# Kernel tuning notes

Measured on AMD Instinct MI355X. Metric: run time of the kernel, lower is better.

## Reference

```python
import jax, jax.numpy as jnp
import numpy as np

B, N, C, H = 8, 2048, 512, 8
D = C // H  # head_dim = 64

def rope(t):
    # t: (B, H, T, D); rotate even/odd interleaved pairs
    T = t.shape[2]
    inv_freq = 1.0 / (10000.0 ** (jnp.arange(0, D, 2, dtype=t.dtype) / D))  # (D/2,)
    pos = jnp.arange(T, dtype=t.dtype)
    freqs = pos[:, None] * inv_freq[None, :]            # (T, D/2)
    cos, sin = jnp.cos(freqs), jnp.sin(freqs)           # broadcast over (B,H)
    t_un = t[..., 0::2]
    t_ev = t[..., 1::2]
    r_un = t_un * cos - t_ev * sin
    r_ev = t_un * sin + t_ev * cos
    # interleave back: (..., D/2, 2) -> (..., D)
    return jnp.stack([r_un, r_ev], axis=-1).reshape(t.shape)

def setup_inputs() -> dict:
    key = jax.random.key(0)
    k1, k2, k3, k4 = jax.random.split(key, 4)
    x = jax.random.normal(k1, (B, N, C), dtype=jnp.float32)
    mask = jax.random.normal(k2, (B, N), dtype=jnp.float32)
    W_qkv = jax.random.normal(k3, (3 * C, C), dtype=jnp.float32) * (1.0 / np.sqrt(C))
    W_proj = jax.random.normal(k4, (C, C), dtype=jnp.float32) * (1.0 / np.sqrt(C))
    b_proj = jnp.zeros((C,), dtype=jnp.float32)
    return {"x": x, "mask": mask, "W_qkv": W_qkv, "W_proj": W_proj,
            "b_proj": b_proj, "num_cls_token": 1}

def reference(x, mask, W_qkv, W_proj, b_proj, num_cls_token):
    scale = D ** (-0.5)
    qkv = jnp.einsum('bnc,fc->bnf', x, W_qkv)             # (B,N,3C)
    qkv = qkv.reshape(B, N, 3, H, D).transpose(2, 0, 3, 1, 4)  # (3,B,H,N,D)
    q, k, v = qkv[0], qkv[1], qkv[2]
    nc = num_cls_token
    if nc > 0:
        q = jnp.concatenate([q[:, :, :nc], rope(q[:, :, nc:])], axis=2)
        k = jnp.concatenate([k[:, :, :nc], rope(k[:, :, nc:])], axis=2)
    else:
        q, k = rope(q), rope(k)
    attn = jnp.einsum('bhnd,bhmd->bhnm', q * scale, k)    # (B,H,N,N)
    attn = attn + mask[:, None, None, :] + mask[:, None, :, None]
    attn = jax.nn.softmax(attn, axis=-1)
    out = jnp.einsum('bhnm,bhmd->bhnd', attn, v)          # (B,H,N,D)
    out = out.transpose(0, 2, 1, 3).reshape(B, N, C)
    return out @ W_proj.T + b_proj
```

## Files before the change

### kernel.cpp

```cpp
#include <hip/hip_runtime.h>
#include <cmath>

#define BB 8
#define NN 2048
#define CC 512
#define HH 8
#define DD 64
#define FF 1536
#define MM (BB*NN)

typedef _Float16 half_t;
typedef __attribute__((ext_vector_type(8))) _Float16 half8;
typedef __attribute__((ext_vector_type(4))) _Float16 half4;
typedef __attribute__((ext_vector_type(4))) float floatx4;
typedef __attribute__((ext_vector_type(16))) float floatx16;
typedef __attribute__((ext_vector_type(4))) float fx4;

#define LOG2E 1.44269504088896f

typedef const __attribute__((address_space(1))) unsigned int* gas_ptr;
typedef __attribute__((address_space(3))) unsigned int* las_ptr;
__device__ __forceinline__ void gld16(const half_t* g, half_t* l) {
  __builtin_amdgcn_global_load_lds((gas_ptr)g, (las_ptr)l, 16, 0, 0);
}

__global__ __launch_bounds__(256) void cvt_kernel(
    const float* __restrict__ s, half_t* __restrict__ d, int n8) {
  int i = blockIdx.x * 256 + threadIdx.x;
  if (i < n8) {
    float4 a = ((const float4*)s)[i * 2], b = ((const float4*)s)[i * 2 + 1];
    half8 h;
    h[0] = (half_t)a.x; h[1] = (half_t)a.y; h[2] = (half_t)a.z; h[3] = (half_t)a.w;
    h[4] = (half_t)b.x; h[5] = (half_t)b.y; h[6] = (half_t)b.z; h[7] = (half_t)b.w;
    ((half8*)d)[i] = h;
  }
}

__global__ __launch_bounds__(256) void qkv_mfma_kernel(
    const half_t* __restrict__ Ah,
    const half_t* __restrict__ Bh,
    const int*   __restrict__ ncp,
    half_t* __restrict__ Qh, half_t* __restrict__ Kh, half_t* __restrict__ Vt)
{
  __shared__ union {
    struct { half_t A[128 * 32]; half_t B[128 * 32]; } s;
    half_t T[4][64 * 68];
  } sm;

  const int tid  = threadIdx.x;
  const int wave = tid >> 6, lane = tid & 63;
  const int L15  = lane & 15, quad = lane >> 4;
  const int wm = (wave & 1) * 64, wn = (wave >> 1) * 64;
  const int m0 = blockIdx.x * 128;
  const int f0 = blockIdx.y * 128;

  const int srow = lane >> 2;
  const int scolh = (lane & 3) * 8;
  const half_t* Ag = Ah + (size_t)(m0 + wave * 16 + srow) * CC + scolh;
  const half_t* Bg = Bh + (size_t)(f0 + wave * 16 + srow) * CC + scolh;
  half_t* Al = &sm.s.A[(wave * 16) * 32];
  half_t* Bl = &sm.s.B[(wave * 16) * 32];

  floatx4 acc[4][4];
#pragma unroll
  for (int i = 0; i < 4; ++i)
#pragma unroll
    for (int j = 0; j < 4; ++j) acc[i][j] = (floatx4){0.f, 0.f, 0.f, 0.f};

  for (int k0 = 0; k0 < CC; k0 += 32) {
    __syncthreads();
    gld16(Ag + k0,            Al);
    gld16(Ag + k0 + 64 * CC,  Al + 64 * 32);
    gld16(Bg + k0,            Bl);
    gld16(Bg + k0 + 64 * CC,  Bl + 64 * 32);
    __syncthreads();
    half8 af[4], bf[4];
#pragma unroll
    for (int mi = 0; mi < 4; ++mi)
      af[mi] = *(const half8*)&sm.s.A[(wm + mi * 16 + L15) * 32 + quad * 8];
#pragma unroll
    for (int ni = 0; ni < 4; ++ni)
      bf[ni] = *(const half8*)&sm.s.B[(wn + ni * 16 + L15) * 32 + quad * 8];
#pragma unroll
    for (int mi = 0; mi < 4; ++mi)
#pragma unroll
      for (int ni = 0; ni < 4; ++ni)
        acc[mi][ni] = __builtin_amdgcn_mfma_f32_16x16x32_f16(af[mi], bf[ni], acc[mi][ni], 0, 0, 0);
  }

  const int which = f0 >> 9;
  const int b     = m0 >> 11;
  const int n_base = (m0 & 2047) + wm;

  if (which < 2) {
    const int nc = *ncp;
    half_t* dst = which ? Kh : Qh;
    const float qscale = which ? 1.0f : (0.125f * LOG2E);
#pragma unroll
    for (int ni = 0; ni < 4; ++ni) {
      const int f = f0 + wn + ni * 16 + L15;
      const int h = (f >> 6) & 7;
      const int d = f & 63;
      const float invf = __powf(10000.0f, -(float)(d & ~1) * (1.0f / 64.0f));
      const float sgn = (d & 1) ? 1.0f : -1.0f;
#pragma unroll
      for (int mi = 0; mi < 4; ++mi)
#pragma unroll
        for (int r = 0; r < 4; ++r) {
          const int n = n_base + mi * 16 + quad * 4 + r;
          float v = acc[mi][ni][r];
          float p = __shfl_xor(v, 1, 64);
          if (n >= nc) {
            float sv, cv;
            __sincosf((float)(n - nc) * invf, &sv, &cv);
            v = v * cv + sgn * p * sv;
          }
          dst[(((size_t)(b * HH + h) * NN + n) << 6) + d] = (half_t)(v * qscale);
        }
    }
  } else {
    __syncthreads();
#pragma unroll
    for (int ni = 0; ni < 4; ++ni)
#pragma unroll
      for (int mi = 0; mi < 4; ++mi)
#pragma unroll
        for (int r = 0; r < 4; ++r)
          sm.T[wave][(ni * 16 + L15) * 68 + mi * 16 + quad * 4 + r] = (half_t)acc[mi][ni][r];
    __syncthreads();
    const int h = ((f0 + wn) >> 6) & 7;
    const size_t gbase = ((size_t)(b * HH + h) * DD + lane) * NN + n_base;
#pragma unroll
    for (int c = 0; c < 8; ++c)
      *(half8*)(Vt + gbase + c * 8) = *(const half8*)&sm.T[wave][lane * 68 + c * 8];
  }
}

#define EXP2_OFF 4.3280851f
__global__ __launch_bounds__(256, 4) void flash_mfma_kernel(
    const half_t* __restrict__ Qh,
    const half_t* __restrict__ Kh,
    const half_t* __restrict__ Vt,
    const float*  __restrict__ mask,
    half_t* __restrict__ O)
{
  __shared__ half_t KV[2][2][64 * 64];

  const int tid  = threadIdx.x;
  const int wave = tid >> 6;
  const int lane = tid & 63;
  const int l31  = lane & 31;
  const int hi   = lane >> 5;
  const int l7   = lane & 7;

  const int bid  = blockIdx.x;
  const int xcd  = bid & 7;
  const int slot = bid >> 3;
  const int qt   = slot & 15;
  const int head = (slot >> 4) * 8 + xcd;
  const int b    = head >> 3;
  const int h    = head & 7;

  const half_t* Kt_base = Kh + ((((size_t)b * HH + h) * NN) << 6);
  const half_t* Vt_base = Vt + (((size_t)b * HH + h) * DD) * NN;

  half8 qf[4];
  {
    const half_t* Qp =
        Qh + ((((size_t)b * HH + h) * NN + qt * 128 + wave * 32 + l31) << 6) + hi * 8;
#pragma unroll
    for (int kd = 0; kd < 4; ++kd) qf[kd] = *(const half8*)(Qp + kd * 16);
  }

  const int r8  = lane >> 3;
  const int dof = ((l7 ^ r8) << 3);
  const half_t* kbase = Kt_base + (((size_t)(wave * 16 + r8)) << 6) + dof;
  const half_t* vbase = Vt_base + (size_t)(wave * 16 + r8) * NN + dof;

  int adK[4], adV[4];
#pragma unroll
  for (int c = 0; c < 4; ++c) {
    adK[c] = l31 * 128 + ((((c << 1) | hi) ^ l7) << 4);
    adV[c] = 8192 + l31 * 128 + ((((c << 1) | hi) ^ l7) << 4);
  }
  const char* L = (const char*)KV;

  floatx16 acc[2];
#pragma unroll
  for (int dt = 0; dt < 2; ++dt)
#pragma unroll
    for (int r = 0; r < 16; ++r) acc[dt][r] = 0.f;
  float l_part = 0.f;

  const float* mkb = mask + (size_t)b * NN + hi * 4;

#define STAGE(c, koff, voff)                                                  \
  {                                                                           \
    gld16(kbase + (koff),          &KV[c][0][wave * 1024]);                   \
    gld16(kbase + (koff) + 512,    &KV[c][0][wave * 1024 + 512]);             \
    gld16(vbase + (voff),          &KV[c][1][wave * 1024]);                   \
    gld16(vbase + (voff) + 8 * NN, &KV[c][1][wave * 1024 + 512]);             \
  }

#define COMPUTE(c, moff)                                                      \
  _Pragma("unroll")                                                           \
  for (int t = 0; t < 2; ++t) {                                               \
    fx4 m4[4];                                                                \
    _Pragma("unroll")                                                         \
    for (int r2 = 0; r2 < 4; ++r2)                                            \
      m4[r2] = *(const fx4*)(mkb + (moff) + t * 32 + r2 * 8);                 \
    floatx16 S;                                                               \
    _Pragma("unroll") for (int r = 0; r < 16; ++r) S[r] = 0.f;                \
    __builtin_amdgcn_s_setprio(1);                                            \
    _Pragma("unroll")                                                         \
    for (int kd = 0; kd < 4; ++kd) {                                          \
      half8 kf = *(const half8*)(L + (adK[kd] + (c) * 16384 + t * 4096));     \
      S = __builtin_amdgcn_mfma_f32_32x32x16_f16(kf, qf[kd], S, 0, 0, 0);     \
    }                                                                         \
    __builtin_amdgcn_s_setprio(0);                                            \
    _Pragma("unroll")                                                         \
    for (int r = 0; r < 16; ++r) {                                            \
      float p = __builtin_amdgcn_exp2f(fmaf(m4[r >> 2][r & 3], LOG2E, S[r] - EXP2_OFF)); \
      l_part += p;                                                            \
      S[r] = p;                                                               \
    }                                                                         \
    unsigned W[4][2];                                                         \
    _Pragma("unroll")                                                         \
    for (int r2 = 0; r2 < 4; ++r2)                                            \
      _Pragma("unroll")                                                       \
      for (int u = 0; u < 2; ++u) {                                           \
        union { half_t hh[2]; unsigned w; } pk;                               \
        pk.hh[0] = (half_t)S[r2 * 4 + 2 * u];                                 \
        pk.hh[1] = (half_t)S[r2 * 4 + 2 * u + 1];                             \
        W[r2][u] = pk.w;                                                      \
      }                                                                       \
    _Pragma("unroll")                                                         \
    for (int ksl = 0; ksl < 2; ++ksl) {                                       \
      unsigned A0 = W[2 * ksl][0],     A1 = W[2 * ksl][1];                    \
      unsigned B0 = W[2 * ksl + 1][0], B1 = W[2 * ksl + 1][1];                \
      unsigned pA0 = __shfl_xor(A0, 32, 64), pA1 = __shfl_xor(A1, 32, 64);    \
      unsigned pB0 = __shfl_xor(B0, 32, 64), pB1 = __shfl_xor(B1, 32, 64);    \
      union { unsigned u4[4]; half8 v; } pw;                                  \
      pw.u4[0] = hi ? pB0 : A0;                                               \
      pw.u4[1] = hi ? pB1 : A1;                                               \
      pw.u4[2] = hi ? B0 : pA0;                                               \
      pw.u4[3] = hi ? B1 : pA1;                                               \
      const int ks = t * 2 + ksl;                                             \
      __builtin_amdgcn_s_setprio(1);                                          \
      _Pragma("unroll")                                                       \
      for (int dt = 0; dt < 2; ++dt) {                                        \
        half8 vf = *(const half8*)(L + (adV[ks] + (c) * 16384 + dt * 4096));  \
        acc[dt] = __builtin_amdgcn_mfma_f32_32x32x16_f16(pw.v, vf, acc[dt], 0, 0, 0); \
      }                                                                       \
      __builtin_amdgcn_s_setprio(0);                                          \
    }                                                                         \
  }

  STAGE(0, 0, 0)
  STAGE(1, 4096, 64)
  asm volatile("s_waitcnt vmcnt(4)");
  __builtin_amdgcn_s_barrier();
  __builtin_amdgcn_sched_barrier(0);
  kbase += 8192; vbase += 128;

#pragma unroll 1
  for (int kt2 = 0; kt2 < 15; ++kt2) {
    COMPUTE(0, 0)
    __builtin_amdgcn_sched_barrier(0);
    __builtin_amdgcn_s_barrier();
    STAGE(0, 0, 0)
    asm volatile("s_waitcnt vmcnt(4)");
    __builtin_amdgcn_s_barrier();
    __builtin_amdgcn_sched_barrier(0);

    COMPUTE(1, 64)
    __builtin_amdgcn_sched_barrier(0);
    __builtin_amdgcn_s_barrier();
    STAGE(1, 4096, 64)
    asm volatile("s_waitcnt vmcnt(4)");
    __builtin_amdgcn_s_barrier();
    __builtin_amdgcn_sched_barrier(0);

    kbase += 8192; vbase += 128;
    mkb += 128;
  }

  COMPUTE(0, 0)
  asm volatile("s_waitcnt vmcnt(0)");
  __builtin_amdgcn_s_barrier();
  __builtin_amdgcn_sched_barrier(0);
  COMPUTE(1, 64)

#undef STAGE
#undef COMPUTE

  l_part += __shfl_xor(l_part, 32, 64);

  const size_t orow = (size_t)b * NN + qt * 128 + wave * 32;
#pragma unroll
  for (int r = 0; r < 16; ++r) {
    const int ql  = (r & 3) + 8 * (r >> 2) + 4 * hi;
    const float iv = 1.0f / __shfl(l_part, ql, 64);
    const size_t ro = ((orow + ql) << 9) + (h << 6) + l31;
    O[ro]      = (half_t)(acc[0][r] * iv);
    O[ro + 32] = (half_t)(acc[1][r] * iv);
  }
}

__global__ __launch_bounds__(256) void proj_mfma_kernel(
    const half_t* __restrict__ Ah,
    const half_t* __restrict__ Bh,
    const float* __restrict__ bias,
    float* __restrict__ out)
{
  __shared__ half_t As[128 * 32];
  __shared__ half_t Bs[128 * 32];

  const int tid  = threadIdx.x;
  const int wave = tid >> 6, lane = tid & 63;
  const int L15  = lane & 15, quad = lane >> 4;
  const int wm = (wave & 1) * 64, wn = (wave >> 1) * 64;
  const int m0 = blockIdx.x * 128;
  const int f0 = blockIdx.y * 128;

  const int srow = lane >> 2;
  const int scolh = (lane & 3) * 8;
  const half_t* Ag = Ah + (size_t)(m0 + wave * 16 + srow) * CC + scolh;
  const half_t* Bg = Bh + (size_t)(f0 + wave * 16 + srow) * CC + scolh;
  half_t* Al = &As[(wave * 16) * 32];
  half_t* Bl = &Bs[(wave * 16) * 32];

  floatx4 acc[4][4];
#pragma unroll
  for (int i = 0; i < 4; ++i)
#pragma unroll
    for (int j = 0; j < 4; ++j) acc[i][j] = (floatx4){0.f, 0.f, 0.f, 0.f};

  for (int k0 = 0; k0 < CC; k0 += 32) {
    __syncthreads();
    gld16(Ag + k0,           Al);
    gld16(Ag + k0 + 64 * CC, Al + 64 * 32);
    gld16(Bg + k0,           Bl);
    gld16(Bg + k0 + 64 * CC, Bl + 64 * 32);
    __syncthreads();
    half8 af[4], bf[4];
#pragma unroll
    for (int mi = 0; mi < 4; ++mi)
      af[mi] = *(const half8*)&As[(wm + mi * 16 + L15) * 32 + quad * 8];
#pragma unroll
    for (int ni = 0; ni < 4; ++ni)
      bf[ni] = *(const half8*)&Bs[(wn + ni * 16 + L15) * 32 + quad * 8];
#pragma unroll
    for (int mi = 0; mi < 4; ++mi)
#pragma unroll
      for (int ni = 0; ni < 4; ++ni)
        acc[mi][ni] = __builtin_amdgcn_mfma_f32_16x16x32_f16(af[mi], bf[ni], acc[mi][ni], 0, 0, 0);
  }

#pragma unroll
  for (int ni = 0; ni < 4; ++ni) {
    const int f = f0 + wn + ni * 16 + L15;
    const float bv = bias[f];
#pragma unroll
    for (int mi = 0; mi < 4; ++mi)
#pragma unroll
      for (int r = 0; r < 4; ++r)
        out[(size_t)(m0 + wm + mi * 16 + quad * 4 + r) * CC + f] = acc[mi][ni][r] + bv;
  }
}

extern "C" void kernel_launch(void* const* d_in, const int* in_sizes, int n_in,
                              void* d_out, int out_size, void* d_ws, size_t ws_size,
                              hipStream_t stream) {
  const float* x     = (const float*)d_in[0];
  const float* mask  = (const float*)d_in[1];
  const float* Wqkv  = (const float*)d_in[2];
  const float* Wproj = (const float*)d_in[3];
  const float* bproj = (const float*)d_in[4];
  const int*   ncp   = (const int*)d_in[5];
  float* out = (float*)d_out;

  const size_t per = (size_t)BB * HH * NN * DD;
  half_t* xh  = (half_t*)d_ws;
  half_t* Wqh = xh + (size_t)MM * CC;
  half_t* Wph = Wqh + (size_t)FF * CC;
  half_t* Qh  = Wph + (size_t)CC * CC;
  half_t* Kh  = Qh + per;
  half_t* Vt  = Kh + per;
  half_t* Oh  = Vt + per;

  cvt_kernel<<<dim3(MM * CC / 8 / 256), 256, 0, stream>>>(x, xh, MM * CC / 8);
  cvt_kernel<<<dim3(FF * CC / 8 / 256), 256, 0, stream>>>(Wqkv, Wqh, FF * CC / 8);
  cvt_kernel<<<dim3(CC * CC / 8 / 256), 256, 0, stream>>>(Wproj, Wph, CC * CC / 8);

  qkv_mfma_kernel<<<dim3(MM / 128, FF / 128), 256, 0, stream>>>(xh, Wqh, ncp, Qh, Kh, Vt);
  flash_mfma_kernel<<<dim3(BB * HH * (NN / 128)), 256, 0, stream>>>(Qh, Kh, Vt, mask, Oh);
  proj_mfma_kernel<<<dim3(MM / 128, CC / 128), 256, 0, stream>>>(Oh, Wph, bproj, out);
}
```

Before: 270.8 us.

## Split flash attention KV range across two wave groups and precompute RoPE table

The flash kernel now runs 512 threads per block: two groups of four waves each process alternating 64-key tiles of the KV sequence for the same 128 queries. Their partial accumulators and row sums are merged through LDS at the end, in exchange for single-buffered staging per group with full vmcnt(0) waits. This doubles the waves per query tile to raise parallelism and latency hiding. Separately, RoPE cos/sin values are precomputed into a table by a small kernel, replacing per-element sincos/pow in the QKV epilogue with table loads.

```diff
diff --git a/kernel.cpp b/kernel.cpp
--- a/kernel.cpp
+++ b/kernel.cpp
@@ -36,10 +36,20 @@
   }
 }
 
+__global__ __launch_bounds__(256) void rope_tab_kernel(float2* __restrict__ tab) {
+  int i = blockIdx.x * 256 + threadIdx.x;
+  int p = i >> 5, j = i & 31;
+  float ang = (float)p * __powf(10000.0f, -(float)(2 * j) * (1.0f / 64.0f));
+  float sv, cv;
+  __sincosf(ang, &sv, &cv);
+  tab[i] = make_float2(cv, sv);
+}
+
 __global__ __launch_bounds__(256) void qkv_mfma_kernel(
     const half_t* __restrict__ Ah,
     const half_t* __restrict__ Bh,
     const int*   __restrict__ ncp,
+    const float2* __restrict__ tab,
     half_t* __restrict__ Qh, half_t* __restrict__ Kh, half_t* __restrict__ Vt)
 {
   __shared__ union {
@@ -101,8 +111,8 @@
       const int f = f0 + wn + ni * 16 + L15;
       const int h = (f >> 6) & 7;
       const int d = f & 63;
-      const float invf = __powf(10000.0f, -(float)(d & ~1) * (1.0f / 64.0f));
       const float sgn = (d & 1) ? 1.0f : -1.0f;
+      const float2* tj = tab + (d >> 1);
 #pragma unroll
       for (int mi = 0; mi < 4; ++mi)
 #pragma unroll
@@ -111,9 +121,8 @@
           float v = acc[mi][ni][r];
           float p = __shfl_xor(v, 1, 64);
           if (n >= nc) {
-            float sv, cv;
-            __sincosf((float)(n - nc) * invf, &sv, &cv);
-            v = v * cv + sgn * p * sv;
+            float2 cs = tj[(size_t)(n - nc) * 32];
+            v = v * cs.x + sgn * p * cs.y;
           }
           dst[(((size_t)(b * HH + h) * NN + n) << 6) + d] = (half_t)(v * qscale);
         }
@@ -137,7 +146,7 @@
 }
 
 #define EXP2_OFF 4.3280851f
-__global__ __launch_bounds__(256, 4) void flash_mfma_kernel(
+__global__ __launch_bounds__(512, 8) void flash_mfma_kernel(
     const half_t* __restrict__ Qh,
     const half_t* __restrict__ Kh,
     const half_t* __restrict__ Vt,
@@ -145,9 +154,12 @@
     half_t* __restrict__ O)
 {
   __shared__ half_t KV[2][2][64 * 64];
+  __shared__ float  Ll[128];
 
   const int tid  = threadIdx.x;
   const int wave = tid >> 6;
+  const int wg   = wave & 3;
+  const int grp  = wave >> 2;
   const int lane = tid & 63;
   const int l31  = lane & 31;
   const int hi   = lane >> 5;
@@ -167,21 +179,21 @@
   half8 qf[4];
   {
     const half_t* Qp =
-        Qh + ((((size_t)b * HH + h) * NN + qt * 128 + wave * 32 + l31) << 6) + hi * 8;
+        Qh + ((((size_t)b * HH + h) * NN + qt * 128 + wg * 32 + l31) << 6) + hi * 8;
 #pragma unroll
     for (int kd = 0; kd < 4; ++kd) qf[kd] = *(const half8*)(Qp + kd * 16);
   }
 
   const int r8  = lane >> 3;
   const int dof = ((l7 ^ r8) << 3);
-  const half_t* kbase = Kt_base + (((size_t)(wave * 16 + r8)) << 6) + dof;
-  const half_t* vbase = Vt_base + (size_t)(wave * 16 + r8) * NN + dof;
+  const half_t* kbase = Kt_base + (((size_t)(grp * 64 + wg * 16 + r8)) << 6) + dof;
+  const half_t* vbase = Vt_base + (size_t)(wg * 16 + r8) * NN + grp * 64 + dof;
 
   int adK[4], adV[4];
 #pragma unroll
   for (int c = 0; c < 4; ++c) {
-    adK[c] = l31 * 128 + ((((c << 1) | hi) ^ l7) << 4);
-    adV[c] = 8192 + l31 * 128 + ((((c << 1) | hi) ^ l7) << 4);
+    adK[c] = grp * 16384 + l31 * 128 + ((((c << 1) | hi) ^ l7) << 4);
+    adV[c] = grp * 16384 + 8192 + l31 * 128 + ((((c << 1) | hi) ^ l7) << 4);
   }
   const char* L = (const char*)KV;
 
@@ -192,29 +204,30 @@
     for (int r = 0; r < 16; ++r) acc[dt][r] = 0.f;
   float l_part = 0.f;
 
-  const float* mkb = mask + (size_t)b * NN + hi * 4;
-
-#define STAGE(c, koff, voff)                                                  \
+  const float* mkb = mask + (size_t)b * NN + grp * 64 + hi * 4;
+
+#define STAGE_KV()                                                            \
   {                                                                           \
-    gld16(kbase + (koff),          &KV[c][0][wave * 1024]);                   \
-    gld16(kbase + (koff) + 512,    &KV[c][0][wave * 1024 + 512]);             \
-    gld16(vbase + (voff),          &KV[c][1][wave * 1024]);                   \
-    gld16(vbase + (voff) + 8 * NN, &KV[c][1][wave * 1024 + 512]);             \
-  }
-
-#define COMPUTE(c, moff)                                                      \
+    gld16(kbase,          &KV[grp][0][wg * 1024]);                            \
+    gld16(kbase + 512,    &KV[grp][0][wg * 1024 + 512]);                      \
+    gld16(vbase,          &KV[grp][1][wg * 1024]);                            \
+    gld16(vbase + 8 * NN, &KV[grp][1][wg * 1024 + 512]);                      \
+    kbase += 8192; vbase += 128;                                              \
+  }
+
+#define COMPUTE()                                                             \
   _Pragma("unroll")                                                           \
   for (int t = 0; t < 2; ++t) {                                               \
     fx4 m4[4];                                                                \
     _Pragma("unroll")                                                         \
     for (int r2 = 0; r2 < 4; ++r2)                                            \
-      m4[r2] = *(const fx4*)(mkb + (moff) + t * 32 + r2 * 8);                 \
+      m4[r2] = *(const fx4*)(mkb + t * 32 + r2 * 8);                          \
     floatx16 S;                                                               \
     _Pragma("unroll") for (int r = 0; r < 16; ++r) S[r] = 0.f;                \
     __builtin_amdgcn_s_setprio(1);                                            \
     _Pragma("unroll")                                                         \
     for (int kd = 0; kd < 4; ++kd) {                                          \
-      half8 kf = *(const half8*)(L + (adK[kd] + (c) * 16384 + t * 4096));     \
+      half8 kf = *(const half8*)(L + (adK[kd] + t * 4096));                   \
       S = __builtin_amdgcn_mfma_f32_32x32x16_f16(kf, qf[kd], S, 0, 0, 0);     \
     }                                                                         \
     __builtin_amdgcn_s_setprio(0);                                            \
@@ -249,61 +262,62 @@
       __builtin_amdgcn_s_setprio(1);                                          \
       _Pragma("unroll")                                                       \
       for (int dt = 0; dt < 2; ++dt) {                                        \
-        half8 vf = *(const half8*)(L + (adV[ks] + (c) * 16384 + dt * 4096));  \
+        half8 vf = *(const half8*)(L + (adV[ks] + dt * 4096));                \
         acc[dt] = __builtin_amdgcn_mfma_f32_32x32x16_f16(pw.v, vf, acc[dt], 0, 0, 0); \
       }                                                                       \
       __builtin_amdgcn_s_setprio(0);                                          \
     }                                                                         \
   }
 
-  STAGE(0, 0, 0)
-  STAGE(1, 4096, 64)
-  asm volatile("s_waitcnt vmcnt(4)");
-  __builtin_amdgcn_s_barrier();
-  __builtin_amdgcn_sched_barrier(0);
-  kbase += 8192; vbase += 128;
-
-#pragma unroll 1
-  for (int kt2 = 0; kt2 < 15; ++kt2) {
-    COMPUTE(0, 0)
-    __builtin_amdgcn_sched_barrier(0);
-    __builtin_amdgcn_s_barrier();
-    STAGE(0, 0, 0)
-    asm volatile("s_waitcnt vmcnt(4)");
-    __builtin_amdgcn_s_barrier();
-    __builtin_amdgcn_sched_barrier(0);
-
-    COMPUTE(1, 64)
-    __builtin_amdgcn_sched_barrier(0);
-    __builtin_amdgcn_s_barrier();
-    STAGE(1, 4096, 64)
-    asm volatile("s_waitcnt vmcnt(4)");
-    __builtin_amdgcn_s_barrier();
-    __builtin_amdgcn_sched_barrier(0);
-
-    kbase += 8192; vbase += 128;
-    mkb += 128;
-  }
-
-  COMPUTE(0, 0)
+  STAGE_KV()
   asm volatile("s_waitcnt vmcnt(0)");
   __builtin_amdgcn_s_barrier();
   __builtin_amdgcn_sched_barrier(0);
-  COMPUTE(1, 64)
-
-#undef STAGE
+
+#pragma unroll 1
+  for (int s = 0; s < 15; ++s) {
+    COMPUTE()
+    __builtin_amdgcn_sched_barrier(0);
+    __builtin_amdgcn_s_barrier();
+    STAGE_KV()
+    asm volatile("s_waitcnt vmcnt(0)");
+    __builtin_amdgcn_s_barrier();
+    __builtin_amdgcn_sched_barrier(0);
+    mkb += 128;
+  }
+  COMPUTE()
+
+#undef STAGE_KV
 #undef COMPUTE
 
+  __builtin_amdgcn_s_barrier();
   l_part += __shfl_xor(l_part, 32, 64);
 
-  const size_t orow = (size_t)b * NN + qt * 128 + wave * 32;
-#pragma unroll
-  for (int r = 0; r < 16; ++r) {
-    const int ql  = (r & 3) + 8 * (r >> 2) + 4 * hi;
-    const float iv = 1.0f / __shfl(l_part, ql, 64);
-    const size_t ro = ((orow + ql) << 9) + (h << 6) + l31;
-    O[ro]      = (half_t)(acc[0][r] * iv);
-    O[ro + 32] = (half_t)(acc[1][r] * iv);
+  float* Lf = (float*)KV;
+  if (grp) {
+#pragma unroll
+    for (int dt = 0; dt < 2; ++dt)
+#pragma unroll
+      for (int r = 0; r < 16; ++r) {
+        const int ql = (r & 3) + 8 * (r >> 2) + 4 * hi;
+        Lf[wg * 2048 + ql * 64 + dt * 32 + l31] = acc[dt][r];
+      }
+    if (!hi) Ll[wg * 32 + l31] = l_part;
+  }
+  __builtin_amdgcn_s_barrier();
+  if (!grp) {
+    const float lt = l_part + Ll[wg * 32 + l31];
+    const size_t orow = (size_t)b * NN + qt * 128 + wg * 32;
+#pragma unroll
+    for (int r = 0; r < 16; ++r) {
+      const int ql  = (r & 3) + 8 * (r >> 2) + 4 * hi;
+      const float iv = 1.0f / __shfl(lt, ql, 64);
+      const float a0 = acc[0][r] + Lf[wg * 2048 + ql * 64 + l31];
+      const float a1 = acc[1][r] + Lf[wg * 2048 + ql * 64 + 32 + l31];
+      const size_t ro = ((orow + ql) << 9) + (h << 6) + l31;
+      O[ro]      = (half_t)(a0 * iv);
+      O[ro + 32] = (half_t)(a1 * iv);
+    }
   }
 }
 
@@ -388,12 +402,14 @@
   half_t* Kh  = Qh + per;
   half_t* Vt  = Kh + per;
   half_t* Oh  = Vt + per;
-
+  float2* tab = (float2*)(Oh + per);
+
+  rope_tab_kernel<<<dim3(NN * 32 / 256), 256, 0, stream>>>(tab);
   cvt_kernel<<<dim3(MM * CC / 8 / 256), 256, 0, stream>>>(x, xh, MM * CC / 8);
   cvt_kernel<<<dim3(FF * CC / 8 / 256), 256, 0, stream>>>(Wqkv, Wqh, FF * CC / 8);
   cvt_kernel<<<dim3(CC * CC / 8 / 256), 256, 0, stream>>>(Wproj, Wph, CC * CC / 8);
 
-  qkv_mfma_kernel<<<dim3(MM / 128, FF / 128), 256, 0, stream>>>(xh, Wqh, ncp, Qh, Kh, Vt);
-  flash_mfma_kernel<<<dim3(BB * HH * (NN / 128)), 256, 0, stream>>>(Qh, Kh, Vt, mask, Oh);
+  qkv_mfma_kernel<<<dim3(MM / 128, FF / 128), 256, 0, stream>>>(xh, Wqh, ncp, tab, Qh, Kh, Vt);
+  flash_mfma_kernel<<<dim3(BB * HH * (NN / 128)), 512, 0, stream>>>(Qh, Kh, Vt, mask, Oh);
   proj_mfma_kernel<<<dim3(MM / 128, CC / 128), 256, 0, stream>>>(Oh, Wph, bproj, out);
 }
```

Result: slower. 813.9 us (+200.5%).

## Precompute RoPE table and scaled mask; seed S with mask, use permlane32_swap

Applied to the files above, without the earlier changes.

Adds a kernel that precomputes a cos/sin RoPE table, so the QKV epilogue does a table lookup instead of per-element sincos and pow. Adds a mask prep kernel that folds LOG2E and the exp offset into the mask. The flash kernel then initializes the MFMA accumulator with the mask so exp2 needs no extra FMA. The half-wave exchange of P uses permlane32_swap instead of four shuffles and selects, and the row sum is split into four partial sums. The cost is two extra small launches and table reads from global memory.

```diff
diff --git a/kernel.cpp b/kernel.cpp
--- a/kernel.cpp
+++ b/kernel.cpp
@@ -17,6 +17,7 @@
 typedef __attribute__((ext_vector_type(4))) float fx4;
 
 #define LOG2E 1.44269504088896f
+#define EXP2_OFF 4.3280851f
 
 typedef const __attribute__((address_space(1))) unsigned int* gas_ptr;
 typedef __attribute__((address_space(3))) unsigned int* las_ptr;
@@ -36,10 +37,26 @@
   }
 }
 
+__global__ __launch_bounds__(256) void mask_prep_kernel(
+    const float* __restrict__ m, float* __restrict__ d) {
+  int i = blockIdx.x * 256 + threadIdx.x;
+  d[i] = m[i] * LOG2E - EXP2_OFF;
+}
+
+__global__ __launch_bounds__(256) void rope_tab_kernel(float2* __restrict__ tab) {
+  int i = blockIdx.x * 256 + threadIdx.x;
+  int p = i >> 5, j = i & 31;
+  float ang = (float)p * __powf(10000.0f, -(float)(2 * j) * (1.0f / 64.0f));
+  float sv, cv;
+  __sincosf(ang, &sv, &cv);
+  tab[i] = make_float2(cv, sv);
+}
+
 __global__ __launch_bounds__(256) void qkv_mfma_kernel(
     const half_t* __restrict__ Ah,
     const half_t* __restrict__ Bh,
     const int*   __restrict__ ncp,
+    const float2* __restrict__ tab,
     half_t* __restrict__ Qh, half_t* __restrict__ Kh, half_t* __restrict__ Vt)
 {
   __shared__ union {
@@ -101,8 +118,8 @@
       const int f = f0 + wn + ni * 16 + L15;
       const int h = (f >> 6) & 7;
       const int d = f & 63;
-      const float invf = __powf(10000.0f, -(float)(d & ~1) * (1.0f / 64.0f));
       const float sgn = (d & 1) ? 1.0f : -1.0f;
+      const float2* tj = tab + (d >> 1);
 #pragma unroll
       for (int mi = 0; mi < 4; ++mi)
 #pragma unroll
@@ -111,9 +128,8 @@
           float v = acc[mi][ni][r];
           float p = __shfl_xor(v, 1, 64);
           if (n >= nc) {
-            float sv, cv;
-            __sincosf((float)(n - nc) * invf, &sv, &cv);
-            v = v * cv + sgn * p * sv;
+            float2 cs = tj[(size_t)(n - nc) * 32];
+            v = v * cs.x + sgn * p * cs.y;
           }
           dst[(((size_t)(b * HH + h) * NN + n) << 6) + d] = (half_t)(v * qscale);
         }
@@ -136,12 +152,11 @@
   }
 }
 
-#define EXP2_OFF 4.3280851f
 __global__ __launch_bounds__(256, 4) void flash_mfma_kernel(
     const half_t* __restrict__ Qh,
     const half_t* __restrict__ Kh,
     const half_t* __restrict__ Vt,
-    const float*  __restrict__ mask,
+    const float*  __restrict__ ms,
     half_t* __restrict__ O)
 {
   __shared__ half_t KV[2][2][64 * 64];
@@ -190,9 +205,9 @@
   for (int dt = 0; dt < 2; ++dt)
 #pragma unroll
     for (int r = 0; r < 16; ++r) acc[dt][r] = 0.f;
-  float l_part = 0.f;
-
-  const float* mkb = mask + (size_t)b * NN + hi * 4;
+  float l4[4] = {0.f, 0.f, 0.f, 0.f};
+
+  const float* mkb = ms + (size_t)b * NN + hi * 4;
 
 #define STAGE(c, koff, voff)                                                  \
   {                                                                           \
@@ -205,12 +220,13 @@
 #define COMPUTE(c, moff)                                                      \
   _Pragma("unroll")                                                           \
   for (int t = 0; t < 2; ++t) {                                               \
-    fx4 m4[4];                                                                \
+    floatx16 S;                                                               \
     _Pragma("unroll")                                                         \
-    for (int r2 = 0; r2 < 4; ++r2)                                            \
-      m4[r2] = *(const fx4*)(mkb + (moff) + t * 32 + r2 * 8);                 \
-    floatx16 S;                                                               \
-    _Pragma("unroll") for (int r = 0; r < 16; ++r) S[r] = 0.f;                \
+    for (int r2 = 0; r2 < 4; ++r2) {                                          \
+      fx4 mv = *(const fx4*)(mkb + (moff) + t * 32 + r2 * 8);                 \
+      S[r2 * 4 + 0] = mv[0]; S[r2 * 4 + 1] = mv[1];                           \
+      S[r2 * 4 + 2] = mv[2]; S[r2 * 4 + 3] = mv[3];                           \
+    }                                                                         \
     __builtin_amdgcn_s_setprio(1);                                            \
     _Pragma("unroll")                                                         \
     for (int kd = 0; kd < 4; ++kd) {                                          \
@@ -220,8 +236,8 @@
     __builtin_amdgcn_s_setprio(0);                                            \
     _Pragma("unroll")                                                         \
     for (int r = 0; r < 16; ++r) {                                            \
-      float p = __builtin_amdgcn_exp2f(fmaf(m4[r >> 2][r & 3], LOG2E, S[r] - EXP2_OFF)); \
-      l_part += p;                                                            \
+      float p = __builtin_amdgcn_exp2f(S[r]);                                 \
+      l4[r & 3] += p;                                                         \
       S[r] = p;                                                               \
     }                                                                         \
     unsigned W[4][2];                                                         \
@@ -236,15 +252,14 @@
       }                                                                       \
     _Pragma("unroll")                                                         \
     for (int ksl = 0; ksl < 2; ++ksl) {                                       \
-      unsigned A0 = W[2 * ksl][0],     A1 = W[2 * ksl][1];                    \
-      unsigned B0 = W[2 * ksl + 1][0], B1 = W[2 * ksl + 1][1];                \
-      unsigned pA0 = __shfl_xor(A0, 32, 64), pA1 = __shfl_xor(A1, 32, 64);    \
-      unsigned pB0 = __shfl_xor(B0, 32, 64), pB1 = __shfl_xor(B1, 32, 64);    \
       union { unsigned u4[4]; half8 v; } pw;                                  \
-      pw.u4[0] = hi ? pB0 : A0;                                               \
-      pw.u4[1] = hi ? pB1 : A1;                                               \
-      pw.u4[2] = hi ? B0 : pA0;                                               \
-      pw.u4[3] = hi ? B1 : pA1;                                               \
+      _Pragma("unroll")                                                       \
+      for (int u = 0; u < 2; ++u) {                                           \
+        auto rr = __builtin_amdgcn_permlane32_swap(                           \
+            (int)W[2 * ksl][u], (int)W[2 * ksl + 1][u], false, false);        \
+        pw.u4[u]     = (unsigned)rr[0];                                       \
+        pw.u4[2 + u] = (unsigned)rr[1];                                       \
+      }                                                                       \
       const int ks = t * 2 + ksl;                                             \
       __builtin_amdgcn_s_setprio(1);                                          \
       _Pragma("unroll")                                                       \
@@ -294,6 +309,7 @@
 #undef STAGE
 #undef COMPUTE
 
+  float l_part = (l4[0] + l4[1]) + (l4[2] + l4[3]);
   l_part += __shfl_xor(l_part, 32, 64);
 
   const size_t orow = (size_t)b * NN + qt * 128 + wave * 32;
@@ -388,12 +404,16 @@
   half_t* Kh  = Qh + per;
   half_t* Vt  = Kh + per;
   half_t* Oh  = Vt + per;
-
+  float2* tab = (float2*)(Oh + per);
+  float*  msb = (float*)(tab + (size_t)NN * 32);
+
+  rope_tab_kernel<<<dim3(NN * 32 / 256), 256, 0, stream>>>(tab);
+  mask_prep_kernel<<<dim3(MM / 256), 256, 0, stream>>>(mask, msb);
   cvt_kernel<<<dim3(MM * CC / 8 / 256), 256, 0, stream>>>(x, xh, MM * CC / 8);
   cvt_kernel<<<dim3(FF * CC / 8 / 256), 256, 0, stream>>>(Wqkv, Wqh, FF * CC / 8);
   cvt_kernel<<<dim3(CC * CC / 8 / 256), 256, 0, stream>>>(Wproj, Wph, CC * CC / 8);
 
-  qkv_mfma_kernel<<<dim3(MM / 128, FF / 128), 256, 0, stream>>>(xh, Wqh, ncp, Qh, Kh, Vt);
-  flash_mfma_kernel<<<dim3(BB * HH * (NN / 128)), 256, 0, stream>>>(Qh, Kh, Vt, mask, Oh);
+  qkv_mfma_kernel<<<dim3(MM / 128, FF / 128), 256, 0, stream>>>(xh, Wqh, ncp, tab, Qh, Kh, Vt);
+  flash_mfma_kernel<<<dim3(BB * HH * (NN / 128)), 256, 0, stream>>>(Qh, Kh, Vt, msb, Oh);
   proj_mfma_kernel<<<dim3(MM / 128, CC / 128), 256, 0, stream>>>(Oh, Wph, bproj, out);
 }
```

After: 396.8 us. 1.47x slower.
